# Optimization experiments

Hardware: AMD Instinct MI355X
Metric: run time of the kernel (lower is better)

The kernel has to match this reference:

```python
import jax, jax.numpy as jnp
import numpy as np

EPS = 1e-4
MP_SILU_C = 0.596
RES_T = 0.3
ATTN_T = 0.3
CLIP = 256.0
HEADS = 8


def normalize(x, dim, eps=EPS):
    # matches torch normalize: x / (eps + sqrt(norm.numel()/x.numel()) * ||x||_dim)
    norm = jnp.sqrt(jnp.sum(jnp.square(x.astype(jnp.float32)), axis=dim, keepdims=True))
    alpha = np.sqrt(norm.size / x.size)
    return x / (eps + alpha * norm).astype(x.dtype)


def mp_silu(x):
    return jax.nn.silu(x) / MP_SILU_C


def mp_sum(a, b, t):
    return (a * (1.0 - t) + b * t) / np.sqrt((1.0 - t) ** 2 + t ** 2)


def mp_conv(x, w, gain=1.0):
    # weight-normalized conv / linear (eval mode: no in-place weight copy)
    w = w.astype(jnp.float32)
    w = normalize(w, tuple(range(1, w.ndim)))
    fan = int(np.prod(w.shape[1:]))
    w = w * (gain / np.sqrt(fan))
    w = w.astype(x.dtype)
    if w.ndim == 2:
        return x @ w.T
    return jax.lax.conv_general_dilated(
        x, w, window_strides=(1, 1), padding='SAME',
        dimension_numbers=('NCHW', 'OIHW', 'NCHW'))


def setup_inputs() -> dict:
    key = jax.random.key(0)
    ks = jax.random.split(key, 8)
    return {
        'x': jax.random.normal(ks[0], (16, 256, 32, 32), jnp.float32),
        'emb': jax.random.normal(ks[1], (16, 1024), jnp.float32),
        'w_skip': jax.random.normal(ks[2], (512, 256, 1, 1), jnp.float32),
        'w_res0': jax.random.normal(ks[3], (512, 512, 3, 3), jnp.float32),
        'w_emb': jax.random.normal(ks[4], (512, 1024), jnp.float32),
        'w_res1': jax.random.normal(ks[5], (512, 512, 3, 3), jnp.float32),
        'w_qkv': jax.random.normal(ks[6], (1536, 512, 1, 1), jnp.float32),
        'w_proj': jax.random.normal(ks[7], (512, 512, 1, 1), jnp.float32),
        'emb_gain': jnp.zeros([], jnp.float32),
    }


def reference(x, emb, w_skip, w_res0, w_emb, w_res1, w_qkv, w_proj, emb_gain):
    # flavor='enc', resample_mode='keep'
    x = mp_conv(x, w_skip)          # conv_skip (in!=out)
    x = normalize(x, 1)             # pixel norm over channels
    y = mp_conv(mp_silu(x), w_res0)
    c = mp_conv(emb, w_emb, gain=emb_gain) + 1.0   # [N, C]
    y = mp_silu(y * c[:, :, None, None].astype(y.dtype))
    y = mp_conv(y, w_res1)
    x = mp_sum(x, y, RES_T)
    # QK-normalized self-attention over H*W tokens
    N, C, H, W = x.shape
    ch = C // HEADS
    y = mp_conv(x, w_qkv)                              # [N, 3C, H, W]
    y = y.reshape(N, HEADS, ch, 3, H * W)
    qkv = normalize(y, 2)                              # L2-normalize per-head channels
    q, k, v = qkv[:, :, :, 0, :], qkv[:, :, :, 1, :], qkv[:, :, :, 2, :]
    attn = jax.nn.softmax(
        jnp.einsum('nhcq,nhck->nhqk', q, k) / np.sqrt(ch), axis=3)
    y = jnp.einsum('nhqk,nhck->nhcq', attn, v).reshape(N, C, H, W)
    y = mp_conv(y, w_proj)
    x = mp_sum(x, y, ATTN_T)
    return jnp.clip(x, -CLIP, CLIP)
```

## Files before the change

kernel.cpp:

```cpp
#include <hip/hip_runtime.h>

typedef unsigned short u16;
typedef unsigned int   u32;
typedef __attribute__((ext_vector_type(8))) short bf16x8;
typedef __attribute__((ext_vector_type(4))) float f32x4;
typedef __attribute__((ext_vector_type(4))) int   int4v;

#define DEV static __device__ __forceinline__

DEV u16 f2b(float f){ u32 u = __builtin_bit_cast(u32,f); u = (u + 0x7FFFu + ((u>>16)&1u))>>16; return (u16)u; }
DEV float b2f(u16 h){ return __builtin_bit_cast(float,(u32)h<<16); }
DEV float mpsilu(float t){ return t/(1.f+__expf(-t)) * 1.6778523489932886f; }
DEV u32 cvtpk(float lo, float hi){ u32 r; asm("v_cvt_pk_bf16_f32 %0, %1, %2" : "=v"(r) : "v"(lo), "v"(hi)); return r; }

DEV void gload16(void* l, const void* g){
  __builtin_amdgcn_global_load_lds(
    (const __attribute__((address_space(1))) void*)g,
    (__attribute__((address_space(3))) void*)l, 16, 0, 0);
}

#define OFF_W0B    0ull
#define OFF_W1B    4718592ull
#define OFF_WSKIPB 9437184ull
#define OFF_WQKVB  9699328ull
#define OFF_WPROJB 11272192ull
#define OFF_WEMB   11796480ull
#define OFF_CEMB   13893632ull
#define OFF_XSKIP  13926400ull
#define OFF_YATT   13926400ull
#define OFF_XNORM  47480832ull
#define OFF_QKVRAW 47480832ull
#define OFF_PAD0   97812480ull
#define OFF_Q      97812480ull
#define OFF_PAD1   116752384ull
#define OFF_V      116752384ull
#define OFF_XB     135692288ull
#define OFF_XRESB  169246720ull
#define OFF_K      186023936ull

__global__ __launch_bounds__(256) void k_prep_weights(
    const float* __restrict__ w_skip, const float* __restrict__ w_res0,
    const float* __restrict__ w_emb,  const float* __restrict__ w_res1,
    const float* __restrict__ w_qkv,  const float* __restrict__ w_proj,
    const float* __restrict__ egain, char* __restrict__ ws)
{
  int b = blockIdx.x, tid = threadIdx.x, lane = tid&63, wid = tid>>6;
  const float* src; int fan, mode, o; u16* dstB=nullptr; float* dstF=nullptr; float gain=1.f;
  if(b<512)       { o=b;      src=w_res0+(size_t)o*4608; fan=4608; mode=1; dstB=(u16*)(ws+OFF_W0B); }
  else if(b<1024) { o=b-512;  src=w_res1+(size_t)o*4608; fan=4608; mode=1; dstB=(u16*)(ws+OFF_W1B); }
  else if(b<1536) { o=b-1024; src=w_skip+(size_t)o*256;  fan=256;  mode=0; dstB=(u16*)(ws+OFF_WSKIPB); }
  else if(b<3072) { o=b-1536; src=w_qkv+(size_t)o*512;   fan=512;  mode=0; dstB=(u16*)(ws+OFF_WQKVB); }
  else if(b<3584) { o=b-3072; src=w_proj+(size_t)o*512;  fan=512;  mode=0; dstB=(u16*)(ws+OFF_WPROJB); }
  else            { o=b-3584; src=w_emb+(size_t)o*1024;  fan=1024; mode=2; dstF=(float*)(ws+OFF_WEMB); gain=*egain; }
  float ss=0;
  for(int i=tid;i<fan;i+=256){ float v=src[i]; ss += v*v; }
  for(int i=1;i<64;i<<=1) ss += __shfl_xor(ss,i);
  __shared__ float red[4];
  if(lane==0) red[wid]=ss;
  __syncthreads();
  ss = red[0]+red[1]+red[2]+red[3];
  float scale = gain / (1e-4f*sqrtf((float)fan) + sqrtf(ss));
  for(int i=tid;i<fan;i+=256){
    float v = src[i]*scale;
    if(mode==0) dstB[(size_t)o*fan + i] = f2b(v);
    else if(mode==1){ int c=i/9, tap=i%9; dstB[(size_t)tap*262144 + o*512 + c] = f2b(v); }
    else dstF[(size_t)o*1024 + i] = v;
  }
}

__global__ __launch_bounds__(256) void k_zero_border(char* __restrict__ ws){
  int idx = blockIdx.x*256 + threadIdx.x;
  int4v z = {0,0,0,0};
  for(; idx < 270336; idx += 67584){
    int chunk = idx & 63;
    int rest  = idx >> 6;
    int bp    = rest % 132;
    int rest2 = rest / 132;
    int n     = rest2 & 15;
    int buf   = rest2 >> 4;
    int py, px;
    if(bp < 34){ py=0; px=bp; }
    else if(bp < 68){ py=33; px=bp-34; }
    else if(bp < 100){ py=1+(bp-68); px=0; }
    else { py=1+(bp-100); px=33; }
    char* dst = ws + OFF_PAD0 + (size_t)buf*18939904ull
              + ((size_t)n*1156 + (size_t)py*34 + px)*1024 + (chunk<<4);
    *(int4v*)dst = z;
  }
}

__global__ __launch_bounds__(256) void k_emb(const float* __restrict__ emb,
    const float* __restrict__ wembs, float* __restrict__ cemb)
{
  int gw = (blockIdx.x*256 + threadIdx.x)>>6, lane = threadIdx.x&63;
  int n = gw>>9, o = gw&511;
  const float* e = emb + (size_t)n*1024;
  const float* w = wembs + (size_t)o*1024;
  float s=0;
  for(int i=lane*4;i<1024;i+=256){
    float4 a=*(const float4*)(e+i), b=*(const float4*)(w+i);
    s += a.x*b.x + a.y*b.y + a.z*b.z + a.w*b.w;
  }
  for(int i=1;i<64;i<<=1) s += __shfl_xor(s,i);
  if(lane==0) cemb[n*512+o] = s + 1.0f;
}

__global__ __launch_bounds__(256) void k_cast_x(const float* __restrict__ x, u16* __restrict__ xb){
  __shared__ u16 t[64*257];
  int bid=blockIdx.x, tid=threadIdx.x;
  int n=bid>>4, p0=(bid&15)<<6;
  int p=tid&63, c0=tid>>6;
  for(int c=c0;c<256;c+=4)
    t[p*257+c] = f2b(x[((size_t)((n<<8)+c)<<10) + p0 + p]);
  __syncthreads();
  for(int task=tid;task<2048;task+=256){
    int pp=task>>5, oc=(task&31)<<3;
    union{u16 u[8]; int4v v;} pk;
    #pragma unroll
    for(int i=0;i<8;++i) pk.u[i]=t[pp*257+oc+i];
    *(int4v*)(xb + ((size_t)((n<<10)+p0+pp))*256 + oc) = pk.v;
  }
}

__global__ __launch_bounds__(512) void k_gemm(const u16* __restrict__ A, const u16* __restrict__ Bw,
    int K, int ntiles, int mode, u16* __restrict__ out_b,
    const u16* __restrict__ xresb, float* __restrict__ dout)
{
  __shared__ u16 SH[3*24576];
  int bid=blockIdx.x, tid=threadIdx.x;
  int cpx = gridDim.x>>3;
  bid = (bid&7)*cpx + (bid>>3);
  int per_n = ntiles<<2;
  int n = bid/per_n, rem = bid%per_n, mt = rem/ntiles, nt = rem%ntiles;
  int lane=tid&63, wid=tid>>6, lg=lane>>4, li=lane&15;
  int wm=(wid>>1)<<6, wn=(wid&1)<<6;
  f32x4 acc[4][4];
  f32x4 zz = {0.f,0.f,0.f,0.f};
  #pragma unroll
  for(int i=0;i<4;++i) for(int j=0;j<4;++j) acc[i][j]=zz;

  const char* apc = (const char*)(A + (size_t)(n*1024 + mt*256)*K);
  const char* bpc = (const char*)(Bw + (size_t)(nt*128)*K);
  int a_off[4], b_off[2], lofA[4], lofB[2];
  #pragma unroll
  for(int i=0;i<4;++i){
    int c = tid + (i<<9);
    int r = c>>3, sc = (c&7) ^ (r&7);
    lofA[i] = c<<4;
    a_off[i] = (r*K + sc*8)*2;
  }
  #pragma unroll
  for(int i=0;i<2;++i){
    int c = tid + (i<<9);
    int r = c>>3, sc = (c&7) ^ (r&7);
    lofB[i] = 32768 + (c<<4);
    b_off[i] = (r*K + sc*8)*2;
  }
  char* SB = (char*)SH;
  auto STAGE = [&](int step, int buf){
    int so = step<<7;
    char* base = SB + buf*49152;
    #pragma unroll
    for(int i=0;i<4;++i) gload16(base + lofA[i], apc + a_off[i] + so);
    #pragma unroll
    for(int i=0;i<2;++i) gload16(base + lofB[i], bpc + b_off[i] + so);
  };
  int nsteps = K>>6;
  STAGE(0,0); STAGE(1,1);
  int bufsel = 0;
  for(int t=0;t<nsteps;++t){
    if(t < nsteps-1){ asm volatile("s_waitcnt vmcnt(6)" ::: "memory"); }
    else            { asm volatile("s_waitcnt vmcnt(0)" ::: "memory"); }
    __builtin_amdgcn_s_barrier();
    __builtin_amdgcn_sched_barrier(0);
    if(t+2 < nsteps) STAGE(t+2, (t+2)%3);
    const char* Ab = SB + bufsel*49152;
    const char* Bb = Ab + 32768;
    #pragma unroll
    for(int ks=0;ks<2;++ks){
      bf16x8 a[4], b[4];
      int bo = (lg<<4) + (ks<<6);
      #pragma unroll
      for(int i=0;i<4;++i){ int r = wm + (i<<4) + li; a[i] = *(const bf16x8*)(Ab + r*128 + (bo ^ ((r&7)<<4))); }
      #pragma unroll
      for(int j=0;j<4;++j){ int r = wn + (j<<4) + li; b[j] = *(const bf16x8*)(Bb + r*128 + (bo ^ ((r&7)<<4))); }
      __builtin_amdgcn_s_setprio(1);
      #pragma unroll
      for(int i=0;i<4;++i)
        #pragma unroll
        for(int j=0;j<4;++j)
          acc[i][j] = __builtin_amdgcn_mfma_f32_16x16x32_bf16(a[i], b[j], acc[i][j], 0, 0, 0);
      __builtin_amdgcn_s_setprio(0);
    }
    bufsel = (bufsel==2) ? 0 : bufsel+1;
  }

  int N = ntiles<<7;
  #pragma unroll
  for(int mf=0;mf<4;++mf){
    #pragma unroll
    for(int nf=0;nf<4;++nf){
      int oc = nt*128 + wn + (nf<<4) + li;
      #pragma unroll
      for(int jj=0;jj<4;++jj){
        float v = acc[mf][nf][jj];
        int p = mt*256 + wm + (mf<<4) + (lg<<2) + jj;
        size_t idx = (size_t)(n*1024+p)*N + oc;
        if(mode==1) out_b[idx]=f2b(v);
        else{
          float xr = b2f(xresb[(size_t)(n*1024+p)*512 + oc]);
          float r = (xr*0.7f + v*0.3f)*1.3130643285972254f;
          r = fminf(fmaxf(r,-256.f),256.f);
          dout[((size_t)(n*512+oc)<<10) + p] = r;
        }
      }
    }
  }
}

__global__ __launch_bounds__(256) void k_conv3x3(const u16* __restrict__ inpad, const u16* __restrict__ wt,
    int mode, const float* __restrict__ cemb, const u16* __restrict__ xnormb,
    u16* __restrict__ ypad, u16* __restrict__ xresb)
{
  __shared__ char SB[61440];
  int bid=blockIdx.x, tid=threadIdx.x;
  bid = (bid&7)*64 + (bid>>3);
  int n=bid>>5, rem=bid&31, mt=rem>>2, nt=rem&3;
  int lane=tid&63, wid=tid>>6, lg=lane>>4, li=lane&15;
  int wm=(wid>>1)<<6, wn=(wid&1)<<6;
  int mt4 = mt<<2;
  f32x4 acc[4][4];
  f32x4 zz={0.f,0.f,0.f,0.f};
  #pragma unroll
  for(int i=0;i<4;++i)
    #pragma unroll
    for(int j=0;j<4;++j) acc[i][j]=zz;

  const char* ipc = (const char*)(inpad + (size_t)n*591872);
  const char* wtc = (const char*)wt;
  int abase[4];
  #pragma unroll
  for(int i=0;i<4;++i){ int r = wm + (i<<4) + li; abase[i] = (r>>5)*34 + (r&31); }

  auto STAGE_B = [&](int tap, int kc, int buf){
    int off = tap*524288 + (kc<<7);
    char* base = SB + 28672 + buf*16384;
    #pragma unroll
    for(int i=0;i<4;++i){
      int c = tid + (i<<8);
      int r = c>>3, sc = ((c&7) ^ (r&7))<<4;
      gload16(base + (c<<4), wtc + (nt*128+r)*1024 + sc + off);
    }
  };
  auto STAGE_A = [&](int kcn){
    #pragma unroll
    for(int i=0;i<7;++i){
      int c = tid + (i<<8);
      int slot = c>>3; if(slot>203) slot=203;
      int scol = ((c&7) ^ (slot&7))<<4;
      int py = (slot*241)>>13;
      int px = slot - py*34;
      gload16(SB + (c<<4), ipc + (size_t)((mt4+py)*34+px)*1024 + (kcn<<7) + scol);
    }
  };

  STAGE_A(0);
  STAGE_B(0,0,0);
  asm volatile("s_waitcnt vmcnt(0)" ::: "memory");
  __builtin_amdgcn_s_barrier();

  int bbuf = 0;
  for(int kc=0;kc<8;++kc){
    for(int tap=0;tap<9;++tap){
      if(tap<8){ STAGE_B(tap+1, kc, bbuf^1);
                 asm volatile("s_waitcnt vmcnt(4)" ::: "memory"); }
      else     { asm volatile("s_waitcnt vmcnt(0)" ::: "memory"); }
      __builtin_amdgcn_s_barrier();
      __builtin_amdgcn_sched_barrier(0);
      int dy = (tap*11)>>5;
      int dd = dy*34 + (tap - dy*3);
      const char* Bb = SB + 28672 + bbuf*16384;
      #pragma unroll
      for(int ks=0;ks<2;++ks){
        bf16x8 a[4], b[4];
        int bo = (lg<<4) + (ks<<6);
        #pragma unroll
        for(int i=0;i<4;++i){
          int slot = abase[i] + dd;
          a[i] = *(const bf16x8*)(SB + slot*128 + (bo ^ ((slot&7)<<4)));
        }
        #pragma unroll
        for(int j=0;j<4;++j){ int r = wn + (j<<4) + li; b[j] = *(const bf16x8*)(Bb + r*128 + (bo ^ ((r&7)<<4))); }
        __builtin_amdgcn_s_setprio(1);
        #pragma unroll
        for(int i=0;i<4;++i)
          #pragma unroll
          for(int j=0;j<4;++j)
            acc[i][j] = __builtin_amdgcn_mfma_f32_16x16x32_bf16(a[i], b[j], acc[i][j], 0, 0, 0);
        __builtin_amdgcn_s_setprio(0);
      }
      if(tap<8) bbuf ^= 1;
    }
    if(kc<7){
      __builtin_amdgcn_s_barrier();
      STAGE_A(kc+1);
      STAGE_B(0, kc+1, bbuf^1);
      bbuf ^= 1;
    }
  }

  #pragma unroll
  for(int mf=0;mf<4;++mf){
    #pragma unroll
    for(int nf=0;nf<4;++nf){
      int oc = nt*128 + wn + (nf<<4) + li;
      float ce = (mode==0) ? cemb[n*512+oc] : 0.f;
      #pragma unroll
      for(int jj=0;jj<4;++jj){
        float v = acc[mf][nf][jj];
        int p = mt*128 + wm + (mf<<4) + (lg<<2) + jj;
        int py=p>>5, px=p&31;
        if(mode==0){
          float s = mpsilu(v*ce);
          ypad[((size_t)n*1156 + (size_t)(py+1)*34 + (px+1))*512 + oc] = f2b(s);
        }else{
          size_t ix = (size_t)(n*1024+p)*512 + oc;
          float r = (b2f(xnormb[ix])*0.7f + v*0.3f)*1.3130643285972254f;
          xresb[ix]=f2b(r);
        }
      }
    }
  }
}

__global__ __launch_bounds__(256) void k_pixnorm(const u16* __restrict__ xs,
    u16* __restrict__ xn, u16* __restrict__ pad0)
{
  int tid=threadIdx.x, lane=tid&63, wid=tid>>6;
  for(int p = blockIdx.x*4 + wid; p < 16384; p += gridDim.x*4){
    union{u16 u[8]; int4v v;} in;
    in.v = *(const int4v*)(xs + (size_t)p*512 + lane*8);
    float f[8]; float ss=0.f;
    #pragma unroll
    for(int i=0;i<8;++i){ f[i]=b2f(in.u[i]); ss += f[i]*f[i]; }
    for(int i=1;i<64;i<<=1) ss += __shfl_xor(ss,i);
    float sc = 1.f/(1e-4f + sqrtf(ss)*0.04419417382415922f);
    union{u16 u[8]; int4v v;} on, op;
    #pragma unroll
    for(int i=0;i<8;++i){ float v=f[i]*sc; on.u[i]=f2b(v); op.u[i]=f2b(mpsilu(v)); }
    *(int4v*)(xn + (size_t)p*512 + lane*8) = on.v;
    int n=p>>10, py=(p>>5)&31, px=p&31;
    u16* pd = pad0 + ((size_t)n*1156 + (size_t)(py+1)*34 + (px+1))*512;
    *(int4v*)(pd + lane*8) = op.v;
  }
}

__global__ __launch_bounds__(256) void k_qkv_norm(const u16* __restrict__ raw,
    u16* __restrict__ q, u16* __restrict__ k, u16* __restrict__ v)
{
  __shared__ u16 lraw[8*1536];
  __shared__ float lscale[192];
  int bid=blockIdx.x, tid=threadIdx.x;
  int n=bid>>7, p0=(bid&127)<<3;
  for(int cc=tid; cc<1536; cc+=256){
    int pix=cc/192, off=(cc%192)<<3;
    *(int4v*)(lraw + pix*1536 + off) = *(const int4v*)(raw + ((size_t)((n<<10)+p0+pix))*1536 + off);
  }
  __syncthreads();
  if(tid<192){
    int pix=tid/24, rem=tid%24, h=rem/3, w=rem%3;
    const u16* r = lraw + pix*1536 + h*192 + w;
    float ss=0;
    #pragma unroll
    for(int c=0;c<64;++c){ float f=b2f(r[c*3]); ss += f*f; }
    lscale[tid] = 1.f/(1e-4f + sqrtf(ss)*0.125f);
  }
  __syncthreads();
  for(int t=tid;t<512;t+=256){
    int pix=t>>6, h=(t>>3)&7, oct=(t&7)<<3;
    float sq=lscale[pix*24+h*3+0]*0.18033688011112043f;
    float sk=lscale[pix*24+h*3+1];
    const u16* r = lraw + pix*1536 + h*192;
    union{u16 u[8]; int4v vv;} pq, pk;
    #pragma unroll
    for(int i=0;i<8;++i){ int c=oct+i; pq.u[i]=f2b(b2f(r[3*c+0])*sq); pk.u[i]=f2b(b2f(r[3*c+1])*sk); }
    size_t base = ((size_t)((n<<3)+h)<<10) + p0 + pix;
    *(int4v*)(q + base*64 + oct) = pq.vv;
    *(int4v*)(k + base*64 + oct) = pk.vv;
  }
  for(int t=tid;t<512;t+=256){
    int h=t>>6, c=t&63;
    union{u16 u[8]; int4v vv;} pv;
    #pragma unroll
    for(int pix=0;pix<8;++pix)
      pv.u[pix] = f2b(b2f(lraw[pix*1536 + h*192 + 3*c + 2]) * lscale[pix*24+h*3+2]);
    *(int4v*)(v + (((size_t)((n<<3)+h)<<6) + c)*1024 + p0) = pv.vv;
  }
}

__global__ __launch_bounds__(256) void k_attn(const u16* __restrict__ Q, const u16* __restrict__ Kb,
    const u16* __restrict__ Vb, u16* __restrict__ yatt)
{
  __shared__ char lds[49152];
  __shared__ float alds[4][32];
  int bid=blockIdx.x, tid=threadIdx.x;
  int pair = (bid&7)*16 + (bid>>6);
  int qt = (bid>>3)&7;
  int n=pair>>3, h=pair&7;
  const char* qb = (const char*)(Q  + ((size_t)pair*1024 + qt*128)*64);
  const char* kb = (const char*)(Kb + (size_t)pair*1024*64);
  const char* vb = (const char*)(Vb + (size_t)pair*64*1024);
  int lane=tid&63, wid=tid>>6, lg=lane>>4, li=lane&15;
  int wq=wid<<5;
  char* Pt = lds + 32768;

  #pragma unroll
  for(int i=0;i<4;++i){
    int c = lane + (i<<6);
    int r = wq + (c>>3);
    int sc = ((c&7) ^ (r&7))<<4;
    gload16(Pt + (wq<<7) + (c<<4), qb + (size_t)r*128 + sc);
  }
  asm volatile("s_waitcnt vmcnt(0)" ::: "memory");
  bf16x8 bq[2][2];
  #pragma unroll
  for(int qq=0;qq<2;++qq)
    #pragma unroll
    for(int ks=0;ks<2;++ks){
      int r=wq+(qq<<4)+li; int bo=(lg<<4)+(ks<<6);
      bq[qq][ks]=*(const bf16x8*)(Pt + r*128 + (bo ^ ((r&7)<<4)));
    }
  asm volatile("s_waitcnt lgkmcnt(0)" ::: "memory");
  __builtin_amdgcn_sched_barrier(0);

  auto STAGE = [&](int kt, int buf){
    char* kd = lds + buf*16384;
    #pragma unroll
    for(int i=0;i<2;++i){
      int c = tid + (i<<8);
      int r = c>>3;
      int sc = ((c&7) ^ (r&7))<<4;
      gload16(kd + (c<<4), kb + (size_t)kt*8192 + (r<<7) + sc);
    }
    #pragma unroll
    for(int i=0;i<2;++i){
      int c = tid + (i<<8);
      int r = c>>3;
      int sc = ((c&7) ^ (r&7))<<4;
      gload16(kd + 8192 + (c<<4), vb + (size_t)r*2048 + kt*128 + sc);
    }
  };
  STAGE(0,0);

  f32x4 o0[2][4];
  float m0=-1e30f, m1=-1e30f, l0=0.f, l1=0.f;
  f32x4 zz={0.f,0.f,0.f,0.f};
  #pragma unroll
  for(int i=0;i<2;++i) for(int j=0;j<4;++j) o0[i][j]=zz;

  for(int kt=0;kt<16;++kt){
    asm volatile("s_waitcnt vmcnt(0)" ::: "memory");
    __builtin_amdgcn_s_barrier();
    __builtin_amdgcn_sched_barrier(0);
    if(kt<15) STAGE(kt+1, (kt+1)&1);
    const char* Kt = lds + (kt&1)*16384;
    const char* Vt = Kt + 8192;
    f32x4 s[4][2];
    #pragma unroll
    for(int i=0;i<4;++i){ s[i][0]=zz; s[i][1]=zz; }
    #pragma unroll
    for(int ks=0;ks<2;++ks){
      int bo=(lg<<4)+(ks<<6);
      bf16x8 a[4];
      #pragma unroll
      for(int kk=0;kk<4;++kk){ int r=(kk<<4)+li; a[kk]=*(const bf16x8*)(Kt + r*128 + (bo ^ ((r&7)<<4))); }
      __builtin_amdgcn_s_setprio(1);
      #pragma unroll
      for(int kk=0;kk<4;++kk)
        #pragma unroll
        for(int qq=0;qq<2;++qq)
          s[kk][qq] = __builtin_amdgcn_mfma_f32_16x16x32_bf16(a[kk], bq[qq][ks], s[kk][qq], 0,0,0);
      __builtin_amdgcn_s_setprio(0);
    }
    float pm0=-1e30f, pm1=-1e30f;
    #pragma unroll
    for(int kk=0;kk<4;++kk)
      #pragma unroll
      for(int jj=0;jj<4;++jj){ pm0=fmaxf(pm0,s[kk][0][jj]); pm1=fmaxf(pm1,s[kk][1][jj]); }
    pm0=fmaxf(pm0,__shfl_xor(pm0,16)); pm0=fmaxf(pm0,__shfl_xor(pm0,32));
    pm1=fmaxf(pm1,__shfl_xor(pm1,16)); pm1=fmaxf(pm1,__shfl_xor(pm1,32));
    if(!__all((pm0 <= m0+11.5f) && (pm1 <= m1+11.5f))){
      float mn0=fmaxf(m0,pm0), mn1=fmaxf(m1,pm1);
      float al0=__builtin_amdgcn_exp2f(m0-mn0), al1=__builtin_amdgcn_exp2f(m1-mn1);
      if(lg==0){ alds[wid][li]=al0; alds[wid][16+li]=al1; }
      m0=mn0; m1=mn1; l0*=al0; l1*=al1;
      #pragma unroll
      for(int mf=0;mf<2;++mf)
        #pragma unroll
        for(int jj=0;jj<4;++jj){
          float am = alds[wid][(mf<<4)+(lg<<2)+jj];
          #pragma unroll
          for(int cf=0;cf<4;++cf) o0[mf][cf][jj]*=am;
        }
    }
    float rs0=0.f, rs1=0.f;
    #pragma unroll
    for(int kk=0;kk<4;++kk)
      #pragma unroll
      for(int jj=0;jj<4;++jj){
        float p0=__builtin_amdgcn_exp2f(s[kk][0][jj]-m0); s[kk][0][jj]=p0; rs0+=p0;
        float p1=__builtin_amdgcn_exp2f(s[kk][1][jj]-m1); s[kk][1][jj]=p1; rs1+=p1;
      }
    rs0+=__shfl_xor(rs0,16); rs0+=__shfl_xor(rs0,32);
    rs1+=__shfl_xor(rs1,16); rs1+=__shfl_xor(rs1,32);
    l0+=rs0; l1+=rs1;
    #pragma unroll
    for(int qq=0;qq<2;++qq){
      int q = wq+(qq<<4)+li;
      int rsw = (q&7)<<4;
      #pragma unroll
      for(int kk=0;kk<4;++kk){
        uint2 w;
        w.x = cvtpk(s[kk][qq][0], s[kk][qq][1]);
        w.y = cvtpk(s[kk][qq][2], s[kk][qq][3]);
        int bo = ((kk<<5)+(lg<<3)) ^ rsw;
        *(uint2*)(Pt + q*128 + bo) = w;
      }
    }
    #pragma unroll
    for(int ks=0;ks<2;++ks){
      int bo=(lg<<4)+(ks<<6);
      bf16x8 a[2], b[4];
      #pragma unroll
      for(int i=0;i<2;++i){ int r=wq+(i<<4)+li; a[i]=*(const bf16x8*)(Pt + r*128 + (bo ^ ((r&7)<<4))); }
      #pragma unroll
      for(int j=0;j<4;++j){ int r=(j<<4)+li;    b[j]=*(const bf16x8*)(Vt + r*128 + (bo ^ ((r&7)<<4))); }
      __builtin_amdgcn_s_setprio(1);
      #pragma unroll
      for(int i=0;i<2;++i)
        #pragma unroll
        for(int j=0;j<4;++j)
          o0[i][j] = __builtin_amdgcn_mfma_f32_16x16x32_bf16(a[i], b[j], o0[i][j], 0,0,0);
      __builtin_amdgcn_s_setprio(0);
    }
  }
  if(lg==0){ alds[wid][li]=1.f/l0; alds[wid][16+li]=1.f/l1; }
  #pragma unroll
  for(int mf=0;mf<2;++mf)
    #pragma unroll
    for(int jj=0;jj<4;++jj){
      float rl = alds[wid][(mf<<4)+(lg<<2)+jj];
      int p=(qt<<7)+wq+(mf<<4)+(lg<<2)+jj;
      #pragma unroll
      for(int nf=0;nf<4;++nf){
        int c=(nf<<4)+li;
        yatt[((size_t)(n*1024)+p)*512 + (h<<6) + c] = f2b(o0[mf][nf][jj]*rl);
      }
    }
}

extern "C" void kernel_launch(void* const* d_in, const int* in_sizes, int n_in,
                              void* d_out, int out_size, void* d_ws, size_t ws_size,
                              hipStream_t stream)
{
  (void)in_sizes; (void)n_in; (void)out_size; (void)ws_size;
  const float* x      = (const float*)d_in[0];
  const float* emb    = (const float*)d_in[1];
  const float* w_skip = (const float*)d_in[2];
  const float* w_res0 = (const float*)d_in[3];
  const float* w_emb  = (const float*)d_in[4];
  const float* w_res1 = (const float*)d_in[5];
  const float* w_qkv  = (const float*)d_in[6];
  const float* w_proj = (const float*)d_in[7];
  const float* egain  = (const float*)d_in[8];
  char* ws = (char*)d_ws;
  float* dout = (float*)d_out;

  u16* w0b    = (u16*)(ws+OFF_W0B);
  u16* w1b    = (u16*)(ws+OFF_W1B);
  u16* wskipb = (u16*)(ws+OFF_WSKIPB);
  u16* wqkvb  = (u16*)(ws+OFF_WQKVB);
  u16* wprojb = (u16*)(ws+OFF_WPROJB);
  float* wembs= (float*)(ws+OFF_WEMB);
  float* cemb = (float*)(ws+OFF_CEMB);
  u16* xskipb = (u16*)(ws+OFF_XSKIP);
  u16* yatt   = (u16*)(ws+OFF_YATT);
  u16* xnormb = (u16*)(ws+OFF_XNORM);
  u16* qkvraw = (u16*)(ws+OFF_QKVRAW);
  u16* pad0   = (u16*)(ws+OFF_PAD0);
  u16* qbuf   = (u16*)(ws+OFF_Q);
  u16* pad1   = (u16*)(ws+OFF_PAD1);
  u16* vbuf   = (u16*)(ws+OFF_V);
  u16* xb     = (u16*)(ws+OFF_XB);
  u16* xresb  = (u16*)(ws+OFF_XRESB);
  u16* kbuf   = (u16*)(ws+OFF_K);

  hipLaunchKernelGGL(k_prep_weights, dim3(4096), dim3(256), 0, stream,
                     w_skip, w_res0, w_emb, w_res1, w_qkv, w_proj, egain, ws);
  hipLaunchKernelGGL(k_zero_border, dim3(264), dim3(256), 0, stream, ws);
  hipLaunchKernelGGL(k_emb, dim3(2048), dim3(256), 0, stream, emb, wembs, cemb);
  hipLaunchKernelGGL(k_cast_x, dim3(256), dim3(256), 0, stream, x, xb);
  hipLaunchKernelGGL(k_gemm, dim3(256), dim3(512), 0, stream,
                     xb, wskipb, 256, 4, 1, xskipb, (const u16*)nullptr, (float*)nullptr);
  hipLaunchKernelGGL(k_pixnorm, dim3(1024), dim3(256), 0, stream, xskipb, xnormb, pad0);
  hipLaunchKernelGGL(k_conv3x3, dim3(512), dim3(256), 0, stream,
                     pad0, w0b, 0, cemb, (const u16*)nullptr, pad1, (u16*)nullptr);
  hipLaunchKernelGGL(k_conv3x3, dim3(512), dim3(256), 0, stream,
                     pad1, w1b, 1, (const float*)nullptr, xnormb, (u16*)nullptr, xresb);
  hipLaunchKernelGGL(k_gemm, dim3(768), dim3(512), 0, stream,
                     xresb, wqkvb, 512, 12, 1, qkvraw, (const u16*)nullptr, (float*)nullptr);
  hipLaunchKernelGGL(k_qkv_norm, dim3(2048), dim3(256), 0, stream, qkvraw, qbuf, kbuf, vbuf);
  hipLaunchKernelGGL(k_attn, dim3(1024), dim3(256), 0, stream, qbuf, kbuf, vbuf, yatt);
  hipLaunchKernelGGL(k_gemm, dim3(256), dim3(512), 0, stream,
                     yatt, wprojb, 512, 4, 2, (u16*)nullptr, xresb, dout);
}
```

Measured before the change: 383.9 us.

## Triple-buffer conv3x3 weights, prefetch A fragments, widen attention blocks, fuse border zeroing

The 3x3 conv kernel moves from double to triple buffering of weight tiles in LDS, stages the next K-chunk's input tile during the last tap, and loads A fragments into registers one tap ahead. This removes the extra barrier between chunks and hides LDS read latency. The attention kernel now uses 512-thread blocks covering 256 queries, so each staged K/V tile is shared by twice as many waves. The border-zeroing kernel is folded into the weight-prep launch to save one launch. In exchange, LDS use and register pressure grow, which may lower occupancy.

Result: slower. 466.9 us (+21.6%).

```diff
diff --git a/kernel.cpp b/kernel.cpp
--- a/kernel.cpp
+++ b/kernel.cpp
@@ -45,6 +45,27 @@
     const float* __restrict__ egain, char* __restrict__ ws)
 {
   int b = blockIdx.x, tid = threadIdx.x, lane = tid&63, wid = tid>>6;
+  if(b >= 4096){
+    int idx = (b-4096)*256 + tid;
+    int4v z = {0,0,0,0};
+    for(; idx < 270336; idx += 67584){
+      int chunk = idx & 63;
+      int rest  = idx >> 6;
+      int bp    = rest % 132;
+      int rest2 = rest / 132;
+      int n     = rest2 & 15;
+      int buf   = rest2 >> 4;
+      int py, px;
+      if(bp < 34){ py=0; px=bp; }
+      else if(bp < 68){ py=33; px=bp-34; }
+      else if(bp < 100){ py=1+(bp-68); px=0; }
+      else { py=1+(bp-100); px=33; }
+      char* dst = ws + OFF_PAD0 + (size_t)buf*18939904ull
+                + ((size_t)n*1156 + (size_t)py*34 + px)*1024 + (chunk<<4);
+      *(int4v*)dst = z;
+    }
+    return;
+  }
   const float* src; int fan, mode, o; u16* dstB=nullptr; float* dstF=nullptr; float gain=1.f;
   if(b<512)       { o=b;      src=w_res0+(size_t)o*4608; fan=4608; mode=1; dstB=(u16*)(ws+OFF_W0B); }
   else if(b<1024) { o=b-512;  src=w_res1+(size_t)o*4608; fan=4608; mode=1; dstB=(u16*)(ws+OFF_W1B); }
@@ -68,27 +89,6 @@
   }
 }
 
-__global__ __launch_bounds__(256) void k_zero_border(char* __restrict__ ws){
-  int idx = blockIdx.x*256 + threadIdx.x;
-  int4v z = {0,0,0,0};
-  for(; idx < 270336; idx += 67584){
-    int chunk = idx & 63;
-    int rest  = idx >> 6;
-    int bp    = rest % 132;
-    int rest2 = rest / 132;
-    int n     = rest2 & 15;
-    int buf   = rest2 >> 4;
-    int py, px;
-    if(bp < 34){ py=0; px=bp; }
-    else if(bp < 68){ py=33; px=bp-34; }
-    else if(bp < 100){ py=1+(bp-68); px=0; }
-    else { py=1+(bp-100); px=33; }
-    char* dst = ws + OFF_PAD0 + (size_t)buf*18939904ull
-              + ((size_t)n*1156 + (size_t)py*34 + px)*1024 + (chunk<<4);
-    *(int4v*)dst = z;
-  }
-}
-
 __global__ __launch_bounds__(256) void k_emb(const float* __restrict__ emb,
     const float* __restrict__ wembs, float* __restrict__ cemb)
 {
@@ -222,7 +222,7 @@
     int mode, const float* __restrict__ cemb, const u16* __restrict__ xnormb,
     u16* __restrict__ ypad, u16* __restrict__ xresb)
 {
-  __shared__ char SB[61440];
+  __shared__ char SB[77824];
   int bid=blockIdx.x, tid=threadIdx.x;
   bid = (bid&7)*64 + (bid>>3);
   int n=bid>>5, rem=bid&31, mt=rem>>2, nt=rem&3;
@@ -263,32 +263,46 @@
       gload16(SB + (c<<4), ipc + (size_t)((mt4+py)*34+px)*1024 + (kcn<<7) + scol);
     }
   };
+  bf16x8 ar[2][4];
+  auto LOAD_A = [&](int tap){
+    int dy = (tap*11)>>5;
+    int dd = dy*34 + (tap - dy*3);
+    #pragma unroll
+    for(int ks=0;ks<2;++ks){
+      int bo = (lg<<4) + (ks<<6);
+      #pragma unroll
+      for(int i=0;i<4;++i){
+        int slot = abase[i] + dd;
+        ar[ks][i] = *(const bf16x8*)(SB + slot*128 + (bo ^ ((slot&7)<<4)));
+      }
+    }
+  };
 
   STAGE_A(0);
   STAGE_B(0,0,0);
-  asm volatile("s_waitcnt vmcnt(0)" ::: "memory");
+  STAGE_B(1,0,1);
+  asm volatile("s_waitcnt vmcnt(4)" ::: "memory");
   __builtin_amdgcn_s_barrier();
 
-  int bbuf = 0;
   for(int kc=0;kc<8;++kc){
     for(int tap=0;tap<9;++tap){
-      if(tap<8){ STAGE_B(tap+1, kc, bbuf^1);
-                 asm volatile("s_waitcnt vmcnt(4)" ::: "memory"); }
-      else     { asm volatile("s_waitcnt vmcnt(0)" ::: "memory"); }
-      __builtin_amdgcn_s_barrier();
+      if(kc>0 || tap>0){
+        if(tap==8){ asm volatile("s_waitcnt vmcnt(0) lgkmcnt(0)" ::: "memory"); }
+        else      { asm volatile("s_waitcnt vmcnt(4)" ::: "memory"); }
+        __builtin_amdgcn_s_barrier();
+      }
       __builtin_amdgcn_sched_barrier(0);
-      int dy = (tap*11)>>5;
-      int dd = dy*34 + (tap - dy*3);
-      const char* Bb = SB + 28672 + bbuf*16384;
+      if(tap==8){
+        if(kc<7){ STAGE_A(kc+1); STAGE_B(0,kc+1,0); STAGE_B(1,kc+1,1); }
+      } else if(tap<7){
+        STAGE_B(tap+2, kc, (tap+2)%3);
+      }
+      if(tap==0) LOAD_A(0);
+      const char* Bb = SB + 28672 + (tap%3)*16384;
       #pragma unroll
       for(int ks=0;ks<2;++ks){
-        bf16x8 a[4], b[4];
+        bf16x8 b[4];
         int bo = (lg<<4) + (ks<<6);
-        #pragma unroll
-        for(int i=0;i<4;++i){
-          int slot = abase[i] + dd;
-          a[i] = *(const bf16x8*)(SB + slot*128 + (bo ^ ((slot&7)<<4)));
-        }
         #pragma unroll
         for(int j=0;j<4;++j){ int r = wn + (j<<4) + li; b[j] = *(const bf16x8*)(Bb + r*128 + (bo ^ ((r&7)<<4))); }
         __builtin_amdgcn_s_setprio(1);
@@ -296,16 +310,10 @@
         for(int i=0;i<4;++i)
           #pragma unroll
           for(int j=0;j<4;++j)
-            acc[i][j] = __builtin_amdgcn_mfma_f32_16x16x32_bf16(a[i], b[j], acc[i][j], 0, 0, 0);
+            acc[i][j] = __builtin_amdgcn_mfma_f32_16x16x32_bf16(ar[ks][i], b[j], acc[i][j], 0, 0, 0);
         __builtin_amdgcn_s_setprio(0);
       }
-      if(tap<8) bbuf ^= 1;
-    }
-    if(kc<7){
-      __builtin_amdgcn_s_barrier();
-      STAGE_A(kc+1);
-      STAGE_B(0, kc+1, bbuf^1);
-      bbuf ^= 1;
+      if(tap<8) LOAD_A(tap+1);
     }
   }
 
@@ -398,16 +406,16 @@
   }
 }
 
-__global__ __launch_bounds__(256) void k_attn(const u16* __restrict__ Q, const u16* __restrict__ Kb,
+__global__ __launch_bounds__(512) void k_attn(const u16* __restrict__ Q, const u16* __restrict__ Kb,
     const u16* __restrict__ Vb, u16* __restrict__ yatt)
 {
-  __shared__ char lds[49152];
-  __shared__ float alds[4][32];
+  __shared__ char lds[65536];
+  __shared__ float alds[8][32];
   int bid=blockIdx.x, tid=threadIdx.x;
-  int pair = (bid&7)*16 + (bid>>6);
-  int qt = (bid>>3)&7;
+  int pair = (bid&7)*16 + (bid>>5);
+  int qt2 = (bid>>3)&3;
   int n=pair>>3, h=pair&7;
-  const char* qb = (const char*)(Q  + ((size_t)pair*1024 + qt*128)*64);
+  const char* qb = (const char*)(Q  + ((size_t)pair*1024 + qt2*256)*64);
   const char* kb = (const char*)(Kb + (size_t)pair*1024*64);
   const char* vb = (const char*)(Vb + (size_t)pair*64*1024);
   int lane=tid&63, wid=tid>>6, lg=lane>>4, li=lane&15;
@@ -435,20 +443,10 @@
 
   auto STAGE = [&](int kt, int buf){
     char* kd = lds + buf*16384;
-    #pragma unroll
-    for(int i=0;i<2;++i){
-      int c = tid + (i<<8);
-      int r = c>>3;
-      int sc = ((c&7) ^ (r&7))<<4;
-      gload16(kd + (c<<4), kb + (size_t)kt*8192 + (r<<7) + sc);
-    }
-    #pragma unroll
-    for(int i=0;i<2;++i){
-      int c = tid + (i<<8);
-      int r = c>>3;
-      int sc = ((c&7) ^ (r&7))<<4;
-      gload16(kd + 8192 + (c<<4), vb + (size_t)r*2048 + kt*128 + sc);
-    }
+    { int c = tid; int r = c>>3; int sc = ((c&7) ^ (r&7))<<4;
+      gload16(kd + (c<<4), kb + (size_t)kt*8192 + (r<<7) + sc); }
+    { int c = tid; int r = c>>3; int sc = ((c&7) ^ (r&7))<<4;
+      gload16(kd + 8192 + (c<<4), vb + (size_t)r*2048 + kt*128 + sc); }
   };
   STAGE(0,0);
 
@@ -550,7 +548,7 @@
     #pragma unroll
     for(int jj=0;jj<4;++jj){
       float rl = alds[wid][(mf<<4)+(lg<<2)+jj];
-      int p=(qt<<7)+wq+(mf<<4)+(lg<<2)+jj;
+      int p=(qt2<<8)+wq+(mf<<4)+(lg<<2)+jj;
       #pragma unroll
       for(int nf=0;nf<4;++nf){
         int c=(nf<<4)+li;
@@ -595,9 +593,8 @@
   u16* xresb  = (u16*)(ws+OFF_XRESB);
   u16* kbuf   = (u16*)(ws+OFF_K);
 
-  hipLaunchKernelGGL(k_prep_weights, dim3(4096), dim3(256), 0, stream,
+  hipLaunchKernelGGL(k_prep_weights, dim3(4360), dim3(256), 0, stream,
                      w_skip, w_res0, w_emb, w_res1, w_qkv, w_proj, egain, ws);
-  hipLaunchKernelGGL(k_zero_border, dim3(264), dim3(256), 0, stream, ws);
   hipLaunchKernelGGL(k_emb, dim3(2048), dim3(256), 0, stream, emb, wembs, cemb);
   hipLaunchKernelGGL(k_cast_x, dim3(256), dim3(256), 0, stream, x, xb);
   hipLaunchKernelGGL(k_gemm, dim3(256), dim3(512), 0, stream,
@@ -610,7 +607,7 @@
   hipLaunchKernelGGL(k_gemm, dim3(768), dim3(512), 0, stream,
                      xresb, wqkvb, 512, 12, 1, qkvraw, (const u16*)nullptr, (float*)nullptr);
   hipLaunchKernelGGL(k_qkv_norm, dim3(2048), dim3(256), 0, stream, qkvraw, qbuf, kbuf, vbuf);
-  hipLaunchKernelGGL(k_attn, dim3(1024), dim3(256), 0, stream, qbuf, kbuf, vbuf, yatt);
+  hipLaunchKernelGGL(k_attn, dim3(512), dim3(512), 0, stream, qbuf, kbuf, vbuf, yatt);
   hipLaunchKernelGGL(k_gemm, dim3(256), dim3(512), 0, stream,
                      yatt, wprojb, 512, 4, 2, (u16*)nullptr, xresb, dout);
 }
```
